# Kernel optimization log

Measured on AMD Instinct MI355X. Metric: run time of the kernel, lower is better.

## Reference

```python
import jax, jax.numpy as jnp
import numpy as np

B, H, S, D = 2, 16, 2048, 64

def setup_inputs() -> dict:
    key = jax.random.key(0)
    kq, kk, kv = jax.random.split(key, 3)
    q = jax.random.normal(kq, (B, H, S, D), dtype=jnp.float32)
    k = jax.random.normal(kk, (B, H, S, D), dtype=jnp.float32)
    v = jax.random.normal(kv, (B, H, S, D), dtype=jnp.float32)
    # causal boolean mask, broadcast to (B, H, S, S)
    causal = jnp.tril(jnp.ones((S, S), dtype=bool))
    mask = jnp.broadcast_to(causal, (B, H, S, S))
    return {"q": q, "k": k, "v": v, "mask": mask}


def reference(q, k, v, mask):
    # NOTE: source module does NOT scale by 1/sqrt(d_k); dropout prob is 0.0.
    scores = jnp.einsum("bhqd,bhkd->bhqk", q, k)  # (B,H,Sq,Sk)
    scores = jnp.where(mask, scores, -jnp.inf)     # additive -inf mask, fused
    probs = jax.nn.softmax(scores, axis=-1)
    out = jnp.einsum("bhqk,bhkd->bhqd", probs, v)
    return out
```

## Files before the change

kernel.cpp:

```cpp
#include <hip/hip_runtime.h>
#include <hip/hip_bf16.h>

#define NB 2
#define NH 16
#define SQ 2048
#define DH 64
#define LOG2E 1.44269504088896340736f

typedef _Float16 f16x8 __attribute__((ext_vector_type(8)));
typedef float f32x16 __attribute__((ext_vector_type(16)));
typedef unsigned u32x2 __attribute__((ext_vector_type(2)));
typedef int v2i __attribute__((ext_vector_type(2)));

__device__ __forceinline__ float exp2asm(float x) {
  float r;
  asm("v_exp_f32 %0, %1" : "=v"(r) : "v"(x));
  return r;
}
__device__ __forceinline__ unsigned pkrtz(float a, float b) {
  unsigned r;
  asm("v_cvt_pkrtz_f16_f32 %0, %1, %2" : "=v"(r) : "v"(a), "v"(b));
  return r;
}
__device__ __forceinline__ void gll16(const void* g, void* l) {
  __builtin_amdgcn_global_load_lds(
      (const __attribute__((address_space(1))) void*)g,
      (__attribute__((address_space(3))) void*)l, 16, 0, 0);
}

union AFrag { unsigned u[4]; f16x8 v; };
union H4 { _Float16 h[4]; u32x2 u2; };
union HS { _Float16 h; short s; };

__global__ __launch_bounds__(256) void prep_kv(
    const float* __restrict__ k, const float* __restrict__ v,
    short* __restrict__ kvF) {
  __shared__ short kls[64][72];
  __shared__ short vls[64][72];
  const int tid = threadIdx.x;
  const int t = blockIdx.x;
  const int bh = blockIdx.y;
  const size_t inbase = ((size_t)bh * SQ + t * 64) * DH;
#pragma unroll
  for (int i = 0; i < 4; ++i) {
    int idx = i * 256 + tid;
    int row = idx >> 4;
    int c4 = (idx & 15) << 2;
    float4 kk = *(const float4*)(k + inbase + row * DH + c4);
    H4 p;
    p.h[0] = (_Float16)kk.x; p.h[1] = (_Float16)kk.y;
    p.h[2] = (_Float16)kk.z; p.h[3] = (_Float16)kk.w;
    *(u32x2*)&kls[row][c4] = p.u2;
    float4 vv = *(const float4*)(v + inbase + row * DH + c4);
    HS a0, a1, a2, a3;
    a0.h = (_Float16)vv.x; a1.h = (_Float16)vv.y;
    a2.h = (_Float16)vv.z; a3.h = (_Float16)vv.w;
    vls[c4 + 0][row] = a0.s;
    vls[c4 + 1][row] = a1.s;
    vls[c4 + 2][row] = a2.s;
    vls[c4 + 3][row] = a3.s;
  }
  __syncthreads();
  const size_t ob = ((size_t)bh * 32 + t) * 8192;
#pragma unroll
  for (int half = 0; half < 2; ++half) {
    int g = half * 256 + tid;
    int kt = g >> 8, ks = (g >> 6) & 3, l = g & 63;
    f16x8 kv8 = *(const f16x8*)&kls[kt * 32 + (l & 31)][ks * 16 + (l >> 5) * 8];
    *(f16x8*)(kvF + ob + (size_t)g * 8) = kv8;
    int s = (g >> 7) & 3, pr = (g >> 6) & 1;
    f16x8 vv8 = *(const f16x8*)&vls[pr * 32 + (l & 31)][s * 16 + (l >> 5) * 8];
    *(f16x8*)(kvF + ob + 4096 + (size_t)g * 8) = vv8;
  }
}

__global__ __launch_bounds__(512, 4) void attn_causal_fwd(
    const float* __restrict__ q, const short* __restrict__ kvF,
    float* __restrict__ out) {
  __shared__ short SB[2][16384];

  const int tid = threadIdx.x;
  const int wave = tid >> 6;
  const int lane = tid & 63;
  const int q31 = lane & 31;
  const int h5 = lane >> 5;
  const int wq = wave & 3;
  const int par = wave >> 2;

  const int lid = (int)blockIdx.x;
  const int c = lid & 255;
  const int head = c & 31;
  const int j = c >> 5;
  const int qb = (lid >> 8) ? j : 15 - j;
  const int qbase = qb * 128;
  const size_t base = (size_t)head * SQ * DH;
  const int qrow_w = qbase + wq * 32;
  const int qg = qrow_w + q31;
  const short* kvB = kvF + (size_t)head * 32 * 8192;

  f16x8 qh[4];
#pragma unroll
  for (int ks = 0; ks < 4; ++ks) {
    const float* qp = q + base + (size_t)qg * DH + ks * 16 + h5 * 8;
    float4 a = *(const float4*)qp;
    float4 b = *(const float4*)(qp + 4);
    float f[8] = {a.x, a.y, a.z, a.w, b.x, b.y, b.z, b.w};
    union { _Float16 h[8]; f16x8 v; } fh;
#pragma unroll
    for (int e = 0; e < 8; ++e) fh.h[e] = (_Float16)(f[e] * LOG2E);
    qh[ks] = fh.v;
  }

#define STAGE(ss, nb)                                                       \
  do {                                                                      \
    const char* srcb = (const char*)kvB + (size_t)(ss)*32768;               \
    char* dstb = (char*)&SB[nb][0];                                         \
    _Pragma("unroll") for (int i = 0; i < 4; ++i) {                         \
      gll16(srcb + i * 8192 + tid * 16, dstb + i * 8192 + tid * 16);        \
    }                                                                       \
  } while (0)

  const int nsup = qb + 1;
  STAGE(0, 0);

  f32x16 o0, o1;
#pragma unroll
  for (int r = 0; r < 16; ++r) { o0[r] = 0.f; o1[r] = 0.f; }
  float m_run = -1e30f, l_run = 0.f;

  for (int s = 0; s < nsup; ++s) {
    asm volatile("s_waitcnt vmcnt(0)" ::: "memory");
    __builtin_amdgcn_sched_barrier(0);
    __builtin_amdgcn_s_barrier();
    __builtin_amdgcn_sched_barrier(0);
    if (s + 1 < nsup) STAGE(s + 1, (s + 1) & 1);

    const short* B = &SB[s & 1][par * 8192];
    const int t = 2 * s + par;
    const int kv0 = t * 64;

    if (kv0 <= qrow_w + 31) {
      const int dq = qrow_w + 31 - kv0;
      const int nk = (dq >> 5) ? 2 : 1;

      f32x16 sa[2];
      __builtin_amdgcn_s_setprio(1);
#pragma unroll
      for (int kt = 0; kt < 2; ++kt) {
        if (kt < nk) {
#pragma unroll
          for (int r = 0; r < 16; ++r) sa[kt][r] = 0.f;
#pragma unroll
          for (int ks = 0; ks < 4; ++ks) {
            f16x8 kf = *(const f16x8*)(B + (kt * 4 + ks) * 512 + lane * 8);
            sa[kt] = __builtin_amdgcn_mfma_f32_32x32x16_f16(kf, qh[ks], sa[kt], 0, 0, 0);
          }
        }
      }
      __builtin_amdgcn_s_setprio(0);

#pragma unroll
      for (int kt = 0; kt < 2; ++kt) {
        if (kt < nk && !(kv0 + kt * 32 + 31 <= qrow_w)) {
#pragma unroll
          for (int r = 0; r < 16; ++r) {
            int kvv = kv0 + kt * 32 + (r & 3) + 8 * (r >> 2) + 4 * h5;
            sa[kt][r] = (kvv <= qg) ? sa[kt][r] : -1e30f;
          }
        }
      }

      float mv[16];
#pragma unroll
      for (int r = 0; r < 16; ++r)
        mv[r] = (nk == 2) ? fmaxf(sa[0][r], sa[1][r]) : sa[0][r];
#pragma unroll
      for (int st = 8; st > 0; st >>= 1)
#pragma unroll
        for (int i = 0; i < 8; ++i)
          if (i < st) mv[i] = fmaxf(mv[i], mv[i + st]);
      float mm = fmaxf(mv[0], __shfl_xor(mv[0], 32));
      if (!__all(mm - m_run <= 8.0f)) {
        float mnew = fmaxf(m_run, mm);
        float sc = exp2asm(m_run - mnew);
        l_run *= sc;
        m_run = mnew;
#pragma unroll
        for (int r = 0; r < 16; ++r) {
          float s_r = __shfl(sc, (r & 3) + 8 * (r >> 2) + 4 * h5);
          o0[r] *= s_r;
          o1[r] *= s_r;
        }
      }
#pragma unroll
      for (int kt = 0; kt < 2; ++kt)
        if (kt < nk)
#pragma unroll
          for (int r = 0; r < 16; ++r) sa[kt][r] = exp2asm(sa[kt][r] - m_run);
      float sv[16];
#pragma unroll
      for (int r = 0; r < 16; ++r)
        sv[r] = (nk == 2) ? sa[0][r] + sa[1][r] : sa[0][r];
#pragma unroll
      for (int st = 8; st > 0; st >>= 1)
#pragma unroll
        for (int i = 0; i < 8; ++i)
          if (i < st) sv[i] += sv[i + st];
      l_run += sv[0] + __shfl_xor(sv[0], 32);
      unsigned cpk[2][8];
#pragma unroll
      for (int kt = 0; kt < 2; ++kt)
        if (kt < nk)
#pragma unroll
          for (int i = 0; i < 8; ++i)
            cpk[kt][i] = pkrtz(sa[kt][2 * i], sa[kt][2 * i + 1]);

      __builtin_amdgcn_s_setprio(1);
#pragma unroll
      for (int sg = 0; sg < 4; ++sg) {
        const int kt = sg >> 1;
        if (kt < nk) {
          const int s1 = sg & 1;
          v2i r0 = __builtin_amdgcn_permlane32_swap(
              (int)cpk[kt][s1 * 4 + 0], (int)cpk[kt][s1 * 4 + 2], false, false);
          v2i r1 = __builtin_amdgcn_permlane32_swap(
              (int)cpk[kt][s1 * 4 + 1], (int)cpk[kt][s1 * 4 + 3], false, false);
          AFrag af;
          af.u[0] = (unsigned)r0.x;
          af.u[1] = (unsigned)r1.x;
          af.u[2] = (unsigned)r0.y;
          af.u[3] = (unsigned)r1.y;
          const short* vbase = B + 4096 + sg * 1024;
          f16x8 b0 = *(const f16x8*)(vbase + lane * 8);
          f16x8 b1 = *(const f16x8*)(vbase + 512 + lane * 8);
          o0 = __builtin_amdgcn_mfma_f32_32x32x16_f16(af.v, b0, o0, 0, 0, 0);
          o1 = __builtin_amdgcn_mfma_f32_32x32x16_f16(af.v, b1, o1, 0, 0, 0);
        }
      }
      __builtin_amdgcn_s_setprio(0);
    }
  }

  __syncthreads();
  float* oLDS = (float*)&SB[0][0];
  float* mlLDS = (float*)&SB[1][0];
  if (par == 1) {
#pragma unroll
    for (int r = 0; r < 16; ++r) {
      int qr = (r & 3) + 8 * (r >> 2) + 4 * h5;
      oLDS[(wq * 32 + qr) * 64 + q31] = o0[r];
      oLDS[(wq * 32 + qr) * 64 + 32 + q31] = o1[r];
    }
    if (h5 == 0) {
      mlLDS[wq * 64 + q31] = m_run;
      mlLDS[wq * 64 + 32 + q31] = l_run;
    }
  }
  __syncthreads();
  if (par == 0) {
    float m_o = mlLDS[wq * 64 + q31];
    float l_o = mlLDS[wq * 64 + 32 + q31];
    float m = fmaxf(m_run, m_o);
    float se = exp2asm(m_run - m);
    float so = exp2asm(m_o - m);
    float inv = 1.0f / (l_run * se + l_o * so);
    float fe = se * inv, fo = so * inv;
#pragma unroll
    for (int r = 0; r < 16; ++r) {
      int qr = (r & 3) + 8 * (r >> 2) + 4 * h5;
      float fe_r = __shfl(fe, qr);
      float fo_r = __shfl(fo, qr);
      float v0 = o0[r] * fe_r + oLDS[(wq * 32 + qr) * 64 + q31] * fo_r;
      float v1 = o1[r] * fe_r + oLDS[(wq * 32 + qr) * 64 + 32 + q31] * fo_r;
      float* op = out + base + (size_t)(qrow_w + qr) * DH + q31;
      op[0] = v0;
      op[32] = v1;
    }
  }
}

extern "C" void kernel_launch(void* const* d_in, const int* in_sizes, int n_in,
                              void* d_out, int out_size, void* d_ws, size_t ws_size,
                              hipStream_t stream) {
  const float* q = (const float*)d_in[0];
  const float* k = (const float*)d_in[1];
  const float* v = (const float*)d_in[2];
  float* out = (float*)d_out;
  short* kvF = (short*)d_ws;

  hipLaunchKernelGGL(prep_kv, dim3(SQ / 64, NB * NH), dim3(256), 0, stream,
                     k, v, kvF);
  hipLaunchKernelGGL(attn_causal_fwd, dim3(512), dim3(512), 0, stream,
                     q, kvF, out);
}
```

Baseline: 51.50 us.

## Load K/V fragments directly from global memory instead of LDS double-buffering

```diff
diff --git a/kernel.cpp b/kernel.cpp
--- a/kernel.cpp
+++ b/kernel.cpp
@@ -21,11 +21,6 @@
   unsigned r;
   asm("v_cvt_pkrtz_f16_f32 %0, %1, %2" : "=v"(r) : "v"(a), "v"(b));
   return r;
-}
-__device__ __forceinline__ void gll16(const void* g, void* l) {
-  __builtin_amdgcn_global_load_lds(
-      (const __attribute__((address_space(1))) void*)g,
-      (__attribute__((address_space(3))) void*)l, 16, 0, 0);
 }
 
 union AFrag { unsigned u[4]; f16x8 v; };
@@ -77,7 +72,8 @@
 __global__ __launch_bounds__(512, 4) void attn_causal_fwd(
     const float* __restrict__ q, const short* __restrict__ kvF,
     float* __restrict__ out) {
-  __shared__ short SB[2][16384];
+  __shared__ float oLDS[4][32][64];
+  __shared__ float mlLDS[4][2][32];
 
   const int tid = threadIdx.x;
   const int wave = tid >> 6;
@@ -111,155 +107,140 @@
     qh[ks] = fh.v;
   }
 
-#define STAGE(ss, nb)                                                       \
-  do {                                                                      \
-    const char* srcb = (const char*)kvB + (size_t)(ss)*32768;               \
-    char* dstb = (char*)&SB[nb][0];                                         \
-    _Pragma("unroll") for (int i = 0; i < 4; ++i) {                         \
-      gll16(srcb + i * 8192 + tid * 16, dstb + i * 8192 + tid * 16);        \
-    }                                                                       \
-  } while (0)
-
-  const int nsup = qb + 1;
-  STAGE(0, 0);
-
   f32x16 o0, o1;
 #pragma unroll
   for (int r = 0; r < 16; ++r) { o0[r] = 0.f; o1[r] = 0.f; }
   float m_run = -1e30f, l_run = 0.f;
 
-  for (int s = 0; s < nsup; ++s) {
-    asm volatile("s_waitcnt vmcnt(0)" ::: "memory");
-    __builtin_amdgcn_sched_barrier(0);
-    __builtin_amdgcn_s_barrier();
-    __builtin_amdgcn_sched_barrier(0);
-    if (s + 1 < nsup) STAGE(s + 1, (s + 1) & 1);
-
-    const short* B = &SB[s & 1][par * 8192];
-    const int t = 2 * s + par;
+  const int tmax = (qrow_w + 31) >> 6;
+  for (int t = par; t <= tmax; t += 2) {
     const int kv0 = t * 64;
-
-    if (kv0 <= qrow_w + 31) {
-      const int dq = qrow_w + 31 - kv0;
-      const int nk = (dq >> 5) ? 2 : 1;
-
-      f32x16 sa[2];
-      __builtin_amdgcn_s_setprio(1);
-#pragma unroll
-      for (int kt = 0; kt < 2; ++kt) {
-        if (kt < nk) {
-#pragma unroll
-          for (int r = 0; r < 16; ++r) sa[kt][r] = 0.f;
-#pragma unroll
-          for (int ks = 0; ks < 4; ++ks) {
-            f16x8 kf = *(const f16x8*)(B + (kt * 4 + ks) * 512 + lane * 8);
-            sa[kt] = __builtin_amdgcn_mfma_f32_32x32x16_f16(kf, qh[ks], sa[kt], 0, 0, 0);
-          }
+    const short* C = kvB + (size_t)t * 8192;
+    const int dq = qrow_w + 31 - kv0;
+    const int nk = (dq >= 32) ? 2 : 1;
+
+    f32x16 sa[2];
+    __builtin_amdgcn_s_setprio(1);
+#pragma unroll
+    for (int kt = 0; kt < 2; ++kt) {
+      if (kt < nk) {
+        f16x8 kf[4];
+#pragma unroll
+        for (int ks = 0; ks < 4; ++ks)
+          kf[ks] = *(const f16x8*)(C + (kt * 4 + ks) * 512 + lane * 8);
+#pragma unroll
+        for (int r = 0; r < 16; ++r) sa[kt][r] = 0.f;
+#pragma unroll
+        for (int ks = 0; ks < 4; ++ks)
+          sa[kt] = __builtin_amdgcn_mfma_f32_32x32x16_f16(kf[ks], qh[ks], sa[kt], 0, 0, 0);
+      }
+    }
+    __builtin_amdgcn_s_setprio(0);
+
+    f16x8 bv[4][2];
+#pragma unroll
+    for (int sg = 0; sg < 4; ++sg) {
+      if ((sg >> 1) < nk) {
+        bv[sg][0] = *(const f16x8*)(C + 4096 + sg * 1024 + lane * 8);
+        bv[sg][1] = *(const f16x8*)(C + 4096 + sg * 1024 + 512 + lane * 8);
+      }
+    }
+
+#pragma unroll
+    for (int kt = 0; kt < 2; ++kt) {
+      if (kt < nk && !(kv0 + kt * 32 + 31 <= qrow_w)) {
+#pragma unroll
+        for (int r = 0; r < 16; ++r) {
+          int kvv = kv0 + kt * 32 + (r & 3) + 8 * (r >> 2) + 4 * h5;
+          sa[kt][r] = (kvv <= qg) ? sa[kt][r] : -1e30f;
         }
       }
-      __builtin_amdgcn_s_setprio(0);
-
-#pragma unroll
-      for (int kt = 0; kt < 2; ++kt) {
-        if (kt < nk && !(kv0 + kt * 32 + 31 <= qrow_w)) {
-#pragma unroll
-          for (int r = 0; r < 16; ++r) {
-            int kvv = kv0 + kt * 32 + (r & 3) + 8 * (r >> 2) + 4 * h5;
-            sa[kt][r] = (kvv <= qg) ? sa[kt][r] : -1e30f;
-          }
-        }
-      }
-
-      float mv[16];
-#pragma unroll
-      for (int r = 0; r < 16; ++r)
-        mv[r] = (nk == 2) ? fmaxf(sa[0][r], sa[1][r]) : sa[0][r];
-#pragma unroll
-      for (int st = 8; st > 0; st >>= 1)
+    }
+
+    float mv[16];
+#pragma unroll
+    for (int r = 0; r < 16; ++r)
+      mv[r] = (nk == 2) ? fmaxf(sa[0][r], sa[1][r]) : sa[0][r];
+#pragma unroll
+    for (int st = 8; st > 0; st >>= 1)
+#pragma unroll
+      for (int i = 0; i < 8; ++i)
+        if (i < st) mv[i] = fmaxf(mv[i], mv[i + st]);
+    float mm = fmaxf(mv[0], __shfl_xor(mv[0], 32));
+    if (!__all(mm - m_run <= 8.0f)) {
+      float mnew = fmaxf(m_run, mm);
+      float sc = exp2asm(m_run - mnew);
+      l_run *= sc;
+      m_run = mnew;
+#pragma unroll
+      for (int r = 0; r < 16; ++r) {
+        float s_r = __shfl(sc, (r & 3) + 8 * (r >> 2) + 4 * h5);
+        o0[r] *= s_r;
+        o1[r] *= s_r;
+      }
+    }
+#pragma unroll
+    for (int kt = 0; kt < 2; ++kt)
+      if (kt < nk)
+#pragma unroll
+        for (int r = 0; r < 16; ++r) sa[kt][r] = exp2asm(sa[kt][r] - m_run);
+    float sv[16];
+#pragma unroll
+    for (int r = 0; r < 16; ++r)
+      sv[r] = (nk == 2) ? sa[0][r] + sa[1][r] : sa[0][r];
+#pragma unroll
+    for (int st = 8; st > 0; st >>= 1)
+#pragma unroll
+      for (int i = 0; i < 8; ++i)
+        if (i < st) sv[i] += sv[i + st];
+    l_run += sv[0] + __shfl_xor(sv[0], 32);
+    unsigned cpk[2][8];
+#pragma unroll
+    for (int kt = 0; kt < 2; ++kt)
+      if (kt < nk)
 #pragma unroll
         for (int i = 0; i < 8; ++i)
-          if (i < st) mv[i] = fmaxf(mv[i], mv[i + st]);
-      float mm = fmaxf(mv[0], __shfl_xor(mv[0], 32));
-      if (!__all(mm - m_run <= 8.0f)) {
-        float mnew = fmaxf(m_run, mm);
-        float sc = exp2asm(m_run - mnew);
-        l_run *= sc;
-        m_run = mnew;
-#pragma unroll
-        for (int r = 0; r < 16; ++r) {
-          float s_r = __shfl(sc, (r & 3) + 8 * (r >> 2) + 4 * h5);
-          o0[r] *= s_r;
-          o1[r] *= s_r;
-        }
-      }
-#pragma unroll
-      for (int kt = 0; kt < 2; ++kt)
-        if (kt < nk)
-#pragma unroll
-          for (int r = 0; r < 16; ++r) sa[kt][r] = exp2asm(sa[kt][r] - m_run);
-      float sv[16];
-#pragma unroll
-      for (int r = 0; r < 16; ++r)
-        sv[r] = (nk == 2) ? sa[0][r] + sa[1][r] : sa[0][r];
-#pragma unroll
-      for (int st = 8; st > 0; st >>= 1)
-#pragma unroll
-        for (int i = 0; i < 8; ++i)
-          if (i < st) sv[i] += sv[i + st];
-      l_run += sv[0] + __shfl_xor(sv[0], 32);
-      unsigned cpk[2][8];
-#pragma unroll
-      for (int kt = 0; kt < 2; ++kt)
-        if (kt < nk)
-#pragma unroll
-          for (int i = 0; i < 8; ++i)
-            cpk[kt][i] = pkrtz(sa[kt][2 * i], sa[kt][2 * i + 1]);
-
-      __builtin_amdgcn_s_setprio(1);
-#pragma unroll
-      for (int sg = 0; sg < 4; ++sg) {
-        const int kt = sg >> 1;
-        if (kt < nk) {
-          const int s1 = sg & 1;
-          v2i r0 = __builtin_amdgcn_permlane32_swap(
-              (int)cpk[kt][s1 * 4 + 0], (int)cpk[kt][s1 * 4 + 2], false, false);
-          v2i r1 = __builtin_amdgcn_permlane32_swap(
-              (int)cpk[kt][s1 * 4 + 1], (int)cpk[kt][s1 * 4 + 3], false, false);
-          AFrag af;
-          af.u[0] = (unsigned)r0.x;
-          af.u[1] = (unsigned)r1.x;
-          af.u[2] = (unsigned)r0.y;
-          af.u[3] = (unsigned)r1.y;
-          const short* vbase = B + 4096 + sg * 1024;
-          f16x8 b0 = *(const f16x8*)(vbase + lane * 8);
-          f16x8 b1 = *(const f16x8*)(vbase + 512 + lane * 8);
-          o0 = __builtin_amdgcn_mfma_f32_32x32x16_f16(af.v, b0, o0, 0, 0, 0);
-          o1 = __builtin_amdgcn_mfma_f32_32x32x16_f16(af.v, b1, o1, 0, 0, 0);
-        }
-      }
-      __builtin_amdgcn_s_setprio(0);
-    }
+          cpk[kt][i] = pkrtz(sa[kt][2 * i], sa[kt][2 * i + 1]);
+
+    __builtin_amdgcn_s_setprio(1);
+#pragma unroll
+    for (int sg = 0; sg < 4; ++sg) {
+      const int kt = sg >> 1;
+      if (kt < nk) {
+        const int s1 = sg & 1;
+        v2i r0 = __builtin_amdgcn_permlane32_swap(
+            (int)cpk[kt][s1 * 4 + 0], (int)cpk[kt][s1 * 4 + 2], false, false);
+        v2i r1 = __builtin_amdgcn_permlane32_swap(
+            (int)cpk[kt][s1 * 4 + 1], (int)cpk[kt][s1 * 4 + 3], false, false);
+        AFrag af;
+        af.u[0] = (unsigned)r0.x;
+        af.u[1] = (unsigned)r1.x;
+        af.u[2] = (unsigned)r0.y;
+        af.u[3] = (unsigned)r1.y;
+        o0 = __builtin_amdgcn_mfma_f32_32x32x16_f16(af.v, bv[sg][0], o0, 0, 0, 0);
+        o1 = __builtin_amdgcn_mfma_f32_32x32x16_f16(af.v, bv[sg][1], o1, 0, 0, 0);
+      }
+    }
+    __builtin_amdgcn_s_setprio(0);
   }
 
   __syncthreads();
-  float* oLDS = (float*)&SB[0][0];
-  float* mlLDS = (float*)&SB[1][0];
   if (par == 1) {
 #pragma unroll
     for (int r = 0; r < 16; ++r) {
       int qr = (r & 3) + 8 * (r >> 2) + 4 * h5;
-      oLDS[(wq * 32 + qr) * 64 + q31] = o0[r];
-      oLDS[(wq * 32 + qr) * 64 + 32 + q31] = o1[r];
+      oLDS[wq][qr][q31] = o0[r];
+      oLDS[wq][qr][32 + q31] = o1[r];
     }
     if (h5 == 0) {
-      mlLDS[wq * 64 + q31] = m_run;
-      mlLDS[wq * 64 + 32 + q31] = l_run;
+      mlLDS[wq][0][q31] = m_run;
+      mlLDS[wq][1][q31] = l_run;
     }
   }
   __syncthreads();
   if (par == 0) {
-    float m_o = mlLDS[wq * 64 + q31];
-    float l_o = mlLDS[wq * 64 + 32 + q31];
+    float m_o = mlLDS[wq][0][q31];
+    float l_o = mlLDS[wq][1][q31];
     float m = fmaxf(m_run, m_o);
     float se = exp2asm(m_run - m);
     float so = exp2asm(m_o - m);
@@ -270,8 +251,8 @@
       int qr = (r & 3) + 8 * (r >> 2) + 4 * h5;
       float fe_r = __shfl(fe, qr);
       float fo_r = __shfl(fo, qr);
-      float v0 = o0[r] * fe_r + oLDS[(wq * 32 + qr) * 64 + q31] * fo_r;
-      float v1 = o1[r] * fe_r + oLDS[(wq * 32 + qr) * 64 + 32 + q31] * fo_r;
+      float v0 = o0[r] * fe_r + oLDS[wq][qr][q31] * fo_r;
+      float v1 = o1[r] * fe_r + oLDS[wq][qr][32 + q31] * fo_r;
       float* op = out + base + (size_t)(qrow_w + qr) * DH + q31;
       op[0] = v0;
       op[32] = v1;
```

New measurement: 96.78 us. 1.88x slower.
